# Performance work log

Measured on AMD Instinct MI355X. Metric: run time of the kernel, lower is better.

The kernel has to match this reference:

```python
import jax, jax.numpy as jnp
import numpy as np

TAPS = 5
DELAY = 3
ITERATIONS = 2
EPS = 1e-10


def wpe_one_iteration(Y, power, taps=TAPS, delay=DELAY, eps=EPS):
    """One WPE iteration.
    Y: (B, F, C, T) complex STFT signal.
    power: (B, F, T) real power estimate.
    Returns dereverberated signal, same shape as Y.
    """
    B, F, C, T = Y.shape
    inv_pow = 1.0 / jnp.maximum(power, eps)  # (B,F,T)

    # Tap-delayed (Toeplitz-like) stacked signal: Ytil[..., p, d, t] = Y[..., d, t - delay - p]
    Ytil = jnp.stack(
        [jnp.pad(Y[..., : T - delay - p], ((0, 0), (0, 0), (0, 0), (delay + p, 0)))
         for p in range(taps)],
        axis=2,
    )  # (B, F, taps, C, T)

    # Original implementation only accumulates statistics for frames where the
    # full tap window is available: t >= delay + taps - 1.
    valid = (jnp.arange(T) >= delay + taps - 1).astype(power.dtype)
    w = inv_pow * valid  # (B,F,T)

    Psi_w = jnp.conj(Ytil) * w[:, :, None, None, :]  # (B,F,taps,C,T)

    # Power-weighted covariance matrix R[(p,d),(q,e)] and cross-correlation b[(p,d),e]
    R = jnp.einsum('bfpdt,bfqet->bfpdqe', Psi_w, Ytil).reshape(B, F, taps * C, taps * C)
    b = jnp.einsum('bfpdt,bfet->bfpde', Psi_w, Y).reshape(B, F, taps * C, C)

    eye = jnp.eye(taps * C, dtype=R.dtype)
    # Batched per-frequency linear solve for the conjugate filter matrix
    G_conj = jnp.linalg.solve(R + eps * eye, b).reshape(B, F, taps, C, C)

    # reverb tail: sum over taps p and source channels d
    reverb_tail = jnp.einsum('bfpde,bfpdt->bfet', G_conj, Ytil)
    return Y - reverb_tail


def setup_inputs() -> dict:
    key = jax.random.key(0)
    k1, k2 = jax.random.split(key)
    B, T, C, F = 8, 512, 8, 257
    data_real = jax.random.normal(k1, (B, T, C, F), dtype=jnp.float32)
    data_imag = jax.random.normal(k2, (B, T, C, F), dtype=jnp.float32)
    ilens = jnp.full((B,), T, dtype=jnp.int64)
    return {"data_real": data_real, "data_imag": data_imag, "ilens": ilens}


def reference(data_real, data_imag, ilens):
    # data: (B, T, C, F) -> (B, F, C, T)
    data = (data_real + 1j * data_imag).astype(jnp.complex64)
    Y = jnp.transpose(data, (0, 3, 2, 1))  # (B,F,C,T)
    enhanced = Y
    for _ in range(ITERATIONS):
        power = jnp.mean(enhanced.real ** 2 + enhanced.imag ** 2, axis=-2)  # (B,F,T)
        enhanced = wpe_one_iteration(Y, power)
        # NOTE: original code calls `enhanced.masked_fill(...)` (non in-place),
        # whose result is discarded -> it is a no-op; ilens here are all == T anyway.
    enhanced = jnp.transpose(enhanced, (0, 3, 2, 1))  # (B,T,C,F)
    # Return real/imag stacked so output is a real float tensor (B,T,C,F,2)
    return jnp.stack([enhanced.real, enhanced.imag], axis=-1)
```

## Files before the change

kernel.cpp:

```cpp
#include <hip/hip_runtime.h>

constexpr int BB = 8;
constexpr int TT = 512;
constexpr int CHN = 8;
constexpr int FF = 257;
constexpr int TAPS = 5;
constexpr int DELAY = 3;
constexpr int NBF = BB * FF;
constexpr int ROWQ = 20;
constexpr int MC = 48;
constexpr int RS = 98;

typedef short s8v __attribute__((ext_vector_type(8)));
typedef float f4  __attribute__((ext_vector_type(4)));

__global__ void k_pack(const float* __restrict__ re, const float* __restrict__ im,
                       float* __restrict__ Yg, float* __restrict__ pw) {
  const int ft = blockIdx.x, tt = blockIdx.y, b = blockIdx.z;
  const int f0 = ft * 32, t0 = tt * 16;
  __shared__ float ls[32 * 258];
  const int tid = threadIdx.x;
  const int l = tid & 31;
  const int r = tid >> 5;
  const int f = f0 + l;
  if (f < FF) {
    for (int k = 0; k < 32; ++k) {
      const int task = r + 8 * k;
      const int ri = task & 1;
      const int c  = (task >> 1) & 7;
      const int t  = task >> 4;
      const float* src = ri ? im : re;
      const float v = src[(((size_t)b * TT + t0 + t) * CHN + c) * FF + f];
      ls[l * 258 + (t * 16 + c * 2 + ri)] = v;
    }
  }
  __syncthreads();
  for (int ff = 0; ff < 32; ++ff) {
    const int fg = f0 + ff;
    if (fg >= FF) break;
    Yg[(((size_t)b * FF + fg) * TT + t0) * 16 + tid] = ls[ff * 258 + tid];
  }
  if (f < FF) {
#pragma unroll
    for (int s = 0; s < 2; ++s) {
      const int t = (tid >> 5) + 8 * s;
      const float* row = &ls[l * 258 + t * 16];
      float ss = 0.f;
#pragma unroll
      for (int q = 0; q < 8; ++q) {
        const float2 v = *(const float2*)&row[q * 2];
        ss += v.x * v.x + v.y * v.y;
      }
      pw[((size_t)b * FF + f) * TT + t0 + t] = ss * (1.0f / CHN);
    }
  }
}

__device__ __forceinline__ unsigned bf16rn(float x) {
  unsigned b = __float_as_uint(x);
  return (b + 0x7fffu + ((b >> 16) & 1u)) >> 16;
}

__global__ __launch_bounds__(384, 4)
void k_corr(const float* __restrict__ Yg,
            const float* __restrict__ pw,
            float2* __restrict__ Mg) {
  const int bf = blockIdx.x;
  __shared__ float pre[512 * 9];
  __shared__ float pim[512 * 9];
  __shared__ unsigned short tiles[4 * 1920];
  const int tid = threadIdx.x;

  for (int t = tid; t < TT; t += 384) {
    const float p = pw[(size_t)bf * TT + t];
    pre[t * 9 + 8] = (t >= DELAY + TAPS - 1) ? rsqrtf(fmaxf(p, 1e-10f)) : 0.0f;
  }
  const float4* ybase4 = (const float4*)(Yg + (size_t)bf * TT * 16);
  for (int fi = tid; fi < TT * 4; fi += 384) {
    const int t = fi >> 2, q = fi & 3;
    const float4 v = ybase4[fi];
    pre[t * 9 + 2 * q] = v.x; pre[t * 9 + 2 * q + 1] = v.z;
    pim[t * 9 + 2 * q] = v.y; pim[t * 9 + 2 * q + 1] = v.w;
  }
  __syncthreads();

  const int lane = tid & 63, wv = tid >> 6;
  const int rt = (wv < 3) ? 0 : (wv < 5 ? 1 : 2);
  const int ct = (wv < 3) ? wv : (wv < 5 ? wv - 2 : 2);
  const int lr = lane & 15, lk = lane >> 4;
  const int aoff = (rt * 16 + lr) * 40 + lk * 8;
  const int boff = (ct * 16 + lr) * 40 + lk * 8;

  f4 accre  = {0.f, 0.f, 0.f, 0.f};
  f4 accim1 = {0.f, 0.f, 0.f, 0.f};
  f4 accim2 = {0.f, 0.f, 0.f, 0.f};

  for (int kt = 0; kt < 16; ++kt) {
    const int kt0 = kt * 32;
#pragma unroll
    for (int cc = 0; cc < 2; ++cc) {
      const int c = tid + cc * 384;
      const int kp = c & 15, row = c >> 4;
      const int t = kt0 + 2 * kp;
      const int sh = (row < 40) ? (DELAY + (row >> 3)) : 0;
      const int e  = (row < 40) ? (row & 7) : (row - 40);
      int s0 = t - sh;     if (s0 < 0) s0 = 0;
      int s1 = t + 1 - sh; if (s1 < 0) s1 = 0;
      const float u0 = pre[t * 9 + 8], u1 = pre[(t + 1) * 9 + 8];
      const float v0r = u0 * pre[s0 * 9 + e], v0i = u0 * pim[s0 * 9 + e];
      const float v1r = u1 * pre[s1 * 9 + e], v1i = u1 * pim[s1 * 9 + e];
      const int idx = row * 40 + 2 * kp;
      {
        const unsigned b0 = __float_as_uint(v0r), b1 = __float_as_uint(v1r);
        *(unsigned*)&tiles[idx] = (b0 >> 16) | (b1 & 0xffff0000u);
        *(unsigned*)&tiles[1920 + idx] =
            bf16rn(v0r - __uint_as_float(b0 & 0xffff0000u)) |
            (bf16rn(v1r - __uint_as_float(b1 & 0xffff0000u)) << 16);
      }
      {
        const unsigned b0 = __float_as_uint(v0i), b1 = __float_as_uint(v1i);
        *(unsigned*)&tiles[3840 + idx] = (b0 >> 16) | (b1 & 0xffff0000u);
        *(unsigned*)&tiles[5760 + idx] =
            bf16rn(v0i - __uint_as_float(b0 & 0xffff0000u)) |
            (bf16rn(v1i - __uint_as_float(b1 & 0xffff0000u)) << 16);
      }
    }
    __syncthreads();
    const s8v crhA = *(const s8v*)&tiles[aoff];
    const s8v crlA = *(const s8v*)&tiles[1920 + aoff];
    const s8v cihA = *(const s8v*)&tiles[3840 + aoff];
    const s8v cilA = *(const s8v*)&tiles[5760 + aoff];
    const s8v crhB = *(const s8v*)&tiles[boff];
    const s8v crlB = *(const s8v*)&tiles[1920 + boff];
    const s8v cihB = *(const s8v*)&tiles[3840 + boff];
    const s8v cilB = *(const s8v*)&tiles[5760 + boff];
    accre  = __builtin_amdgcn_mfma_f32_16x16x32_bf16(crhA, crhB, accre, 0, 0, 0);
    accre  = __builtin_amdgcn_mfma_f32_16x16x32_bf16(crlA, crhB, accre, 0, 0, 0);
    accre  = __builtin_amdgcn_mfma_f32_16x16x32_bf16(crhA, crlB, accre, 0, 0, 0);
    accre  = __builtin_amdgcn_mfma_f32_16x16x32_bf16(cihA, cihB, accre, 0, 0, 0);
    accre  = __builtin_amdgcn_mfma_f32_16x16x32_bf16(cilA, cihB, accre, 0, 0, 0);
    accre  = __builtin_amdgcn_mfma_f32_16x16x32_bf16(cihA, cilB, accre, 0, 0, 0);
    accim1 = __builtin_amdgcn_mfma_f32_16x16x32_bf16(crhA, cihB, accim1, 0, 0, 0);
    accim1 = __builtin_amdgcn_mfma_f32_16x16x32_bf16(crlA, cihB, accim1, 0, 0, 0);
    accim1 = __builtin_amdgcn_mfma_f32_16x16x32_bf16(crhA, cilB, accim1, 0, 0, 0);
    accim2 = __builtin_amdgcn_mfma_f32_16x16x32_bf16(cihA, crhB, accim2, 0, 0, 0);
    accim2 = __builtin_amdgcn_mfma_f32_16x16x32_bf16(cilA, crhB, accim2, 0, 0, 0);
    accim2 = __builtin_amdgcn_mfma_f32_16x16x32_bf16(cihA, crlB, accim2, 0, 0, 0);
    __syncthreads();
  }

#pragma unroll
  for (int r = 0; r < 4; ++r) {
    const int i = rt * 16 + lk * 4 + r;
    const int j = ct * 16 + lr;
    const float revl = accre[r];
    const float imvl = accim1[r] - accim2[r];
    if (i < 40) {
      float rr = revl;
      if (i == j) rr += 1e-10f;
      Mg[((size_t)bf * 40 + i) * MC + j] = make_float2(rr, imvl);
    }
    if (rt < ct && j < 40) {
      Mg[((size_t)bf * 40 + j) * MC + i] = make_float2(revl, -imvl);
    }
  }
}

__global__ __launch_bounds__(128) void k_solve(const float2* __restrict__ Mg,
                                               float2* __restrict__ Gg) {
  const int bf = blockIdx.x;
  __shared__ float ml[40 * RS];
  const int tid = threadIdx.x;
  for (int idx = tid; idx < 40 * MC; idx += 128) {
    const int i = idx / MC, j = idx - i * MC;
    float2 v = Mg[((size_t)bf * 40 + i) * MC + j];
    *(float2*)&ml[i * RS + j * 2] = v;
  }
  __syncthreads();
  const int li = tid >> 3, lj = tid & 7;
  for (int k = 0; k < 40; ++k) {
    const float inr = __builtin_amdgcn_rcpf(ml[k * RS + k * 2]);
    for (int i = k + 1 + li; i < 40; i += 16) {
      const float2 aik = *(float2*)&ml[i * RS + k * 2];
      const float fr = aik.x * inr;
      const float fi = aik.y * inr;
      for (int j = k + 1 + lj; j < MC; j += 8) {
        const float2 ak = *(float2*)&ml[k * RS + j * 2];
        float2 ai = *(float2*)&ml[i * RS + j * 2];
        ai.x -= fr * ak.x - fi * ak.y;
        ai.y -= fr * ak.y + fi * ak.x;
        *(float2*)&ml[i * RS + j * 2] = ai;
      }
    }
    __syncthreads();
  }
  const int lane = tid & 63, wave = tid >> 6;
  const int e = 4 * wave + (lane & 3), cc = lane >> 2;
  for (int k = 39; k >= 0; --k) {
    float sr = 0.f, si = 0.f;
    for (int j = k + 1 + cc; j < 40; j += 16) {
      const float2 u = *(float2*)&ml[k * RS + j * 2];
      const float2 x = *(float2*)&ml[j * RS + (40 + e) * 2];
      sr += u.x * x.x - u.y * x.y;
      si += u.x * x.y + u.y * x.x;
    }
    sr += __shfl_xor(sr, 4);  si += __shfl_xor(si, 4);
    sr += __shfl_xor(sr, 8);  si += __shfl_xor(si, 8);
    sr += __shfl_xor(sr, 16); si += __shfl_xor(si, 16);
    sr += __shfl_xor(sr, 32); si += __shfl_xor(si, 32);
    if (cc == 0) {
      const float inr = __builtin_amdgcn_rcpf(ml[k * RS + k * 2]);
      const float2 rhs = *(float2*)&ml[k * RS + (40 + e) * 2];
      *(float2*)&ml[k * RS + (40 + e) * 2] =
          make_float2((rhs.x - sr) * inr, (rhs.y - si) * inr);
    }
    asm volatile("" ::: "memory");
  }
  __syncthreads();
  for (int idx = tid; idx < 320; idx += 128) {
    const int i = idx >> 3, ee = idx & 7;
    Gg[(size_t)bf * 320 + idx] = *(float2*)&ml[i * RS + (40 + ee) * 2];
  }
}

template <int MODE>
__global__ __launch_bounds__(256) void k_tail(float* __restrict__ Yg,
                                              const float2* __restrict__ Gg,
                                              float* __restrict__ pw) {
  const int bf = blockIdx.x;
  __shared__ float yl[TT * ROWQ];
  __shared__ float gl[640];
  const int tid = threadIdx.x;
  for (int idx = tid; idx < 320; idx += 256) {
    float2 g = Gg[(size_t)bf * 320 + idx];
    *(float2*)&gl[idx * 2] = g;
  }
  const float4* ybase4 = (const float4*)(Yg + (size_t)bf * TT * 16);
  for (int fi = tid; fi < TT * 4; fi += 256) {
    const int row = fi >> 2, wq = fi & 3;
    *((float4*)&yl[row * ROWQ + wq * 4]) = ybase4[fi];
  }
  __syncthreads();

  const int t0 = tid;
  const int t1 = tid + 256;
  float acc[2][16];
  {
    const float* yr0 = &yl[t0 * ROWQ];
    const float* yr1 = &yl[t1 * ROWQ];
#pragma unroll
    for (int q = 0; q < 16; ++q) { acc[0][q] = yr0[q]; acc[1][q] = yr1[q]; }
  }
#pragma unroll 1
  for (int p = 0; p < TAPS; ++p) {
    const int rp0 = t0 - DELAY - p;
    const int rp1 = t1 - DELAY - p;
    const float* yrow0 = &yl[(rp0 >= 0 ? rp0 : 0) * ROWQ];
    const float* yrow1 = &yl[rp1 * ROWQ];
    const float m0 = (rp0 >= 0) ? 1.0f : 0.0f;
    const float* gp = &gl[p * 128];
#pragma unroll
    for (int d = 0; d < CHN; ++d) {
      const float y0r = m0 * yrow0[2 * d], y0i = m0 * yrow0[2 * d + 1];
      const float y1r = yrow1[2 * d],      y1i = yrow1[2 * d + 1];
      const float4 g0 = *(const float4*)&gp[d * 16 + 0];
      const float4 g1 = *(const float4*)&gp[d * 16 + 4];
      const float4 g2 = *(const float4*)&gp[d * 16 + 8];
      const float4 g3 = *(const float4*)&gp[d * 16 + 12];
      const float gr[8] = {g0.x, g0.z, g1.x, g1.z, g2.x, g2.z, g3.x, g3.z};
      const float gi[8] = {g0.y, g0.w, g1.y, g1.w, g2.y, g2.w, g3.y, g3.w};
#pragma unroll
      for (int ee = 0; ee < 8; ++ee) {
        acc[0][2 * ee]     -= gr[ee] * y0r - gi[ee] * y0i;
        acc[0][2 * ee + 1] -= gr[ee] * y0i + gi[ee] * y0r;
        acc[1][2 * ee]     -= gr[ee] * y1r - gi[ee] * y1i;
        acc[1][2 * ee + 1] -= gr[ee] * y1i + gi[ee] * y1r;
      }
    }
  }
  float* ybase = Yg + (size_t)bf * TT * 16;
  if (MODE == 0) {
#pragma unroll
    for (int s = 0; s < 2; ++s) {
      const int t = tid + s * 256;
      float ss = 0.f;
#pragma unroll
      for (int q = 0; q < 16; ++q) ss += acc[s][q] * acc[s][q];
      pw[(size_t)bf * TT + t] = ss * (1.0f / CHN);
    }
  } else {
#pragma unroll
    for (int s = 0; s < 2; ++s) {
      const int t = tid + s * 256;
      float4* dst = (float4*)(ybase + (size_t)t * 16);
      dst[0] = make_float4(acc[s][0], acc[s][1], acc[s][2], acc[s][3]);
      dst[1] = make_float4(acc[s][4], acc[s][5], acc[s][6], acc[s][7]);
      dst[2] = make_float4(acc[s][8], acc[s][9], acc[s][10], acc[s][11]);
      dst[3] = make_float4(acc[s][12], acc[s][13], acc[s][14], acc[s][15]);
    }
  }
}

__global__ void k_unpack(const float* __restrict__ Yg, float* __restrict__ out) {
  const int ft = blockIdx.x, tt = blockIdx.y, b = blockIdx.z;
  const int f0 = ft * 32, t0 = tt * 16;
  __shared__ float ls[32 * 258];
  const int tid = threadIdx.x;
  for (int ff = 0; ff < 32; ++ff) {
    const int fg = f0 + ff;
    if (fg >= FF) break;
    ls[ff * 258 + tid] = Yg[(((size_t)b * FF + fg) * TT + t0) * 16 + tid];
  }
  __syncthreads();
  const int l = tid & 31, r = tid >> 5;
  const int fg = f0 + l;
  if (fg < FF) {
    for (int k = 0; k < 16; ++k) {
      const int task = r + 8 * k;
      const int t = task >> 3, c = task & 7;
      const float2 v = *(float2*)&ls[l * 258 + t * 16 + c * 2];
      *(float2*)&out[((((size_t)b * TT + t0 + t) * CHN + c) * FF + fg) * 2] = v;
    }
  }
}

extern "C" void kernel_launch(void* const* d_in, const int* in_sizes, int n_in,
                              void* d_out, int out_size, void* d_ws, size_t ws_size,
                              hipStream_t stream) {
  const float* re = (const float*)d_in[0];
  const float* im = (const float*)d_in[1];
  float* ws = (float*)d_ws;

  float*  Yg = ws;
  float*  pw = Yg + (size_t)NBF * TT * 16;
  float2* Mg = (float2*)(pw + (size_t)NBF * TT);
  float2* Gg = Mg + (size_t)NBF * 40 * MC;
  float*  out = (float*)d_out;

  const dim3 gridT(9, 32, BB);
  k_pack<<<gridT, 256, 0, stream>>>(re, im, Yg, pw);

  for (int iter = 0; iter < 2; ++iter) {
    k_corr<<<NBF, 384, 0, stream>>>(Yg, pw, Mg);
    k_solve<<<NBF, 128, 0, stream>>>(Mg, Gg);
    if (iter == 0)
      k_tail<0><<<NBF, 256, 0, stream>>>(Yg, Gg, pw);
    else
      k_tail<1><<<NBF, 256, 0, stream>>>(Yg, Gg, pw);
  }

  k_unpack<<<gridT, 256, 0, stream>>>(Yg, out);
}
```

Before: 480.0 us.

## Double-buffer correlation tiles and run the solve with a single wave

The correlation kernel now uses two LDS tile buffers and builds the next K-slice while the MFMAs consume the current one, so each iteration needs one barrier instead of two. Its launch-bounds occupancy hint is also dropped. The solve kernel shrinks to one 64-thread wavefront, which lets the per-pivot block barriers become compiler memory fences, with the shuffle reduction adjusted to match. The costs are more LDS per correlation block, possibly lower occupancy, and half as many threads doing the elimination work.

```diff
diff --git a/kernel.cpp b/kernel.cpp
--- a/kernel.cpp
+++ b/kernel.cpp
@@ -61,14 +61,14 @@
   return (b + 0x7fffu + ((b >> 16) & 1u)) >> 16;
 }
 
-__global__ __launch_bounds__(384, 4)
+__global__ __launch_bounds__(384)
 void k_corr(const float* __restrict__ Yg,
             const float* __restrict__ pw,
             float2* __restrict__ Mg) {
   const int bf = blockIdx.x;
   __shared__ float pre[512 * 9];
   __shared__ float pim[512 * 9];
-  __shared__ unsigned short tiles[4 * 1920];
+  __shared__ unsigned short tiles[2 * 7680];
   const int tid = threadIdx.x;
 
   for (int t = tid; t < TT; t += 384) {
@@ -82,21 +82,8 @@
     pre[t * 9 + 2 * q] = v.x; pre[t * 9 + 2 * q + 1] = v.z;
     pim[t * 9 + 2 * q] = v.y; pim[t * 9 + 2 * q + 1] = v.w;
   }
-  __syncthreads();
-
-  const int lane = tid & 63, wv = tid >> 6;
-  const int rt = (wv < 3) ? 0 : (wv < 5 ? 1 : 2);
-  const int ct = (wv < 3) ? wv : (wv < 5 ? wv - 2 : 2);
-  const int lr = lane & 15, lk = lane >> 4;
-  const int aoff = (rt * 16 + lr) * 40 + lk * 8;
-  const int boff = (ct * 16 + lr) * 40 + lk * 8;
-
-  f4 accre  = {0.f, 0.f, 0.f, 0.f};
-  f4 accim1 = {0.f, 0.f, 0.f, 0.f};
-  f4 accim2 = {0.f, 0.f, 0.f, 0.f};
-
-  for (int kt = 0; kt < 16; ++kt) {
-    const int kt0 = kt * 32;
+
+  auto build = [&](int kt0, unsigned short* tb) {
 #pragma unroll
     for (int cc = 0; cc < 2; ++cc) {
       const int c = tid + cc * 384;
@@ -112,28 +99,46 @@
       const int idx = row * 40 + 2 * kp;
       {
         const unsigned b0 = __float_as_uint(v0r), b1 = __float_as_uint(v1r);
-        *(unsigned*)&tiles[idx] = (b0 >> 16) | (b1 & 0xffff0000u);
-        *(unsigned*)&tiles[1920 + idx] =
+        *(unsigned*)&tb[idx] = (b0 >> 16) | (b1 & 0xffff0000u);
+        *(unsigned*)&tb[1920 + idx] =
             bf16rn(v0r - __uint_as_float(b0 & 0xffff0000u)) |
             (bf16rn(v1r - __uint_as_float(b1 & 0xffff0000u)) << 16);
       }
       {
         const unsigned b0 = __float_as_uint(v0i), b1 = __float_as_uint(v1i);
-        *(unsigned*)&tiles[3840 + idx] = (b0 >> 16) | (b1 & 0xffff0000u);
-        *(unsigned*)&tiles[5760 + idx] =
+        *(unsigned*)&tb[3840 + idx] = (b0 >> 16) | (b1 & 0xffff0000u);
+        *(unsigned*)&tb[5760 + idx] =
             bf16rn(v0i - __uint_as_float(b0 & 0xffff0000u)) |
             (bf16rn(v1i - __uint_as_float(b1 & 0xffff0000u)) << 16);
       }
     }
-    __syncthreads();
-    const s8v crhA = *(const s8v*)&tiles[aoff];
-    const s8v crlA = *(const s8v*)&tiles[1920 + aoff];
-    const s8v cihA = *(const s8v*)&tiles[3840 + aoff];
-    const s8v cilA = *(const s8v*)&tiles[5760 + aoff];
-    const s8v crhB = *(const s8v*)&tiles[boff];
-    const s8v crlB = *(const s8v*)&tiles[1920 + boff];
-    const s8v cihB = *(const s8v*)&tiles[3840 + boff];
-    const s8v cilB = *(const s8v*)&tiles[5760 + boff];
+  };
+
+  __syncthreads();
+  build(0, tiles);
+  __syncthreads();
+
+  const int lane = tid & 63, wv = tid >> 6;
+  const int rt = (wv < 3) ? 0 : (wv < 5 ? 1 : 2);
+  const int ct = (wv < 3) ? wv : (wv < 5 ? wv - 2 : 2);
+  const int lr = lane & 15, lk = lane >> 4;
+  const int aoff = (rt * 16 + lr) * 40 + lk * 8;
+  const int boff = (ct * 16 + lr) * 40 + lk * 8;
+
+  f4 accre  = {0.f, 0.f, 0.f, 0.f};
+  f4 accim1 = {0.f, 0.f, 0.f, 0.f};
+  f4 accim2 = {0.f, 0.f, 0.f, 0.f};
+
+  for (int kt = 0; kt < 16; ++kt) {
+    const unsigned short* cur = tiles + (kt & 1) * 7680;
+    const s8v crhA = *(const s8v*)&cur[aoff];
+    const s8v crlA = *(const s8v*)&cur[1920 + aoff];
+    const s8v cihA = *(const s8v*)&cur[3840 + aoff];
+    const s8v cilA = *(const s8v*)&cur[5760 + aoff];
+    const s8v crhB = *(const s8v*)&cur[boff];
+    const s8v crlB = *(const s8v*)&cur[1920 + boff];
+    const s8v cihB = *(const s8v*)&cur[3840 + boff];
+    const s8v cilB = *(const s8v*)&cur[5760 + boff];
     accre  = __builtin_amdgcn_mfma_f32_16x16x32_bf16(crhA, crhB, accre, 0, 0, 0);
     accre  = __builtin_amdgcn_mfma_f32_16x16x32_bf16(crlA, crhB, accre, 0, 0, 0);
     accre  = __builtin_amdgcn_mfma_f32_16x16x32_bf16(crhA, crlB, accre, 0, 0, 0);
@@ -146,6 +151,7 @@
     accim2 = __builtin_amdgcn_mfma_f32_16x16x32_bf16(cihA, crhB, accim2, 0, 0, 0);
     accim2 = __builtin_amdgcn_mfma_f32_16x16x32_bf16(cilA, crhB, accim2, 0, 0, 0);
     accim2 = __builtin_amdgcn_mfma_f32_16x16x32_bf16(cihA, crlB, accim2, 0, 0, 0);
+    if (kt < 15) build((kt + 1) * 32, tiles + ((kt + 1) & 1) * 7680);
     __syncthreads();
   }
 
@@ -166,21 +172,21 @@
   }
 }
 
-__global__ __launch_bounds__(128) void k_solve(const float2* __restrict__ Mg,
-                                               float2* __restrict__ Gg) {
+__global__ __launch_bounds__(64) void k_solve(const float2* __restrict__ Mg,
+                                              float2* __restrict__ Gg) {
   const int bf = blockIdx.x;
   __shared__ float ml[40 * RS];
-  const int tid = threadIdx.x;
-  for (int idx = tid; idx < 40 * MC; idx += 128) {
+  const int lane = threadIdx.x;
+  for (int idx = lane; idx < 40 * MC; idx += 64) {
     const int i = idx / MC, j = idx - i * MC;
     float2 v = Mg[((size_t)bf * 40 + i) * MC + j];
     *(float2*)&ml[i * RS + j * 2] = v;
   }
   __syncthreads();
-  const int li = tid >> 3, lj = tid & 7;
+  const int li = lane >> 3, lj = lane & 7;
   for (int k = 0; k < 40; ++k) {
     const float inr = __builtin_amdgcn_rcpf(ml[k * RS + k * 2]);
-    for (int i = k + 1 + li; i < 40; i += 16) {
+    for (int i = k + 1 + li; i < 40; i += 8) {
       const float2 aik = *(float2*)&ml[i * RS + k * 2];
       const float fr = aik.x * inr;
       const float fi = aik.y * inr;
@@ -192,19 +198,17 @@
         *(float2*)&ml[i * RS + j * 2] = ai;
       }
     }
-    __syncthreads();
-  }
-  const int lane = tid & 63, wave = tid >> 6;
-  const int e = 4 * wave + (lane & 3), cc = lane >> 2;
+    asm volatile("" ::: "memory");
+  }
+  const int e = lane & 7, cc = lane >> 3;
   for (int k = 39; k >= 0; --k) {
     float sr = 0.f, si = 0.f;
-    for (int j = k + 1 + cc; j < 40; j += 16) {
+    for (int j = k + 1 + cc; j < 40; j += 8) {
       const float2 u = *(float2*)&ml[k * RS + j * 2];
       const float2 x = *(float2*)&ml[j * RS + (40 + e) * 2];
       sr += u.x * x.x - u.y * x.y;
       si += u.x * x.y + u.y * x.x;
     }
-    sr += __shfl_xor(sr, 4);  si += __shfl_xor(si, 4);
     sr += __shfl_xor(sr, 8);  si += __shfl_xor(si, 8);
     sr += __shfl_xor(sr, 16); si += __shfl_xor(si, 16);
     sr += __shfl_xor(sr, 32); si += __shfl_xor(si, 32);
@@ -217,7 +221,7 @@
     asm volatile("" ::: "memory");
   }
   __syncthreads();
-  for (int idx = tid; idx < 320; idx += 128) {
+  for (int idx = lane; idx < 320; idx += 64) {
     const int i = idx >> 3, ee = idx & 7;
     Gg[(size_t)bf * 320 + idx] = *(float2*)&ml[i * RS + (40 + ee) * 2];
   }
@@ -342,7 +346,7 @@
 
   for (int iter = 0; iter < 2; ++iter) {
     k_corr<<<NBF, 384, 0, stream>>>(Yg, pw, Mg);
-    k_solve<<<NBF, 128, 0, stream>>>(Mg, Gg);
+    k_solve<<<NBF, 64, 0, stream>>>(Mg, Gg);
     if (iter == 0)
       k_tail<0><<<NBF, 256, 0, stream>>>(Yg, Gg, pw);
     else
```

Result: slower. 561.4 us (+16.9%).

## Fuse per-frequency linear solve into reverb-tail kernel with prefetched Y

Applied to the files above, without the earlier changes.

Merges the separate solve kernel into the tail kernel, so the filter matrix stays in shared memory instead of going through a global Gg buffer. One kernel launch per iteration is removed. The global loads of the Y tile are issued into registers before the elimination starts, so their latency overlaps the solve. The solve now runs with 256 threads and a wider row and column split. The cost is higher shared-memory and register use per block, which may reduce occupancy.

```diff
diff --git a/kernel.cpp b/kernel.cpp
--- a/kernel.cpp
+++ b/kernel.cpp
@@ -166,21 +166,32 @@
   }
 }
 
-__global__ __launch_bounds__(128) void k_solve(const float2* __restrict__ Mg,
-                                               float2* __restrict__ Gg) {
+template <int MODE>
+__global__ __launch_bounds__(256) void k_tailsolve(float* __restrict__ Yg,
+                                                   const float2* __restrict__ Mg,
+                                                   float* __restrict__ pw) {
   const int bf = blockIdx.x;
+  __shared__ float yl[TT * ROWQ];
   __shared__ float ml[40 * RS];
+  __shared__ float gl[640];
   const int tid = threadIdx.x;
-  for (int idx = tid; idx < 40 * MC; idx += 128) {
+
+  const float4* ybase4 = (const float4*)(Yg + (size_t)bf * TT * 16);
+  float4 stage[8];
+#pragma unroll
+  for (int s = 0; s < 8; ++s) stage[s] = ybase4[tid + s * 256];
+
+  for (int idx = tid; idx < 40 * MC; idx += 256) {
     const int i = idx / MC, j = idx - i * MC;
     float2 v = Mg[((size_t)bf * 40 + i) * MC + j];
     *(float2*)&ml[i * RS + j * 2] = v;
   }
   __syncthreads();
+
   const int li = tid >> 3, lj = tid & 7;
   for (int k = 0; k < 40; ++k) {
     const float inr = __builtin_amdgcn_rcpf(ml[k * RS + k * 2]);
-    for (int i = k + 1 + li; i < 40; i += 16) {
+    for (int i = k + 1 + li; i < 40; i += 32) {
       const float2 aik = *(float2*)&ml[i * RS + k * 2];
       const float fr = aik.x * inr;
       const float fi = aik.y * inr;
@@ -194,51 +205,42 @@
     }
     __syncthreads();
   }
-  const int lane = tid & 63, wave = tid >> 6;
-  const int e = 4 * wave + (lane & 3), cc = lane >> 2;
-  for (int k = 39; k >= 0; --k) {
-    float sr = 0.f, si = 0.f;
-    for (int j = k + 1 + cc; j < 40; j += 16) {
-      const float2 u = *(float2*)&ml[k * RS + j * 2];
-      const float2 x = *(float2*)&ml[j * RS + (40 + e) * 2];
-      sr += u.x * x.x - u.y * x.y;
-      si += u.x * x.y + u.y * x.x;
-    }
-    sr += __shfl_xor(sr, 4);  si += __shfl_xor(si, 4);
-    sr += __shfl_xor(sr, 8);  si += __shfl_xor(si, 8);
-    sr += __shfl_xor(sr, 16); si += __shfl_xor(si, 16);
-    sr += __shfl_xor(sr, 32); si += __shfl_xor(si, 32);
-    if (cc == 0) {
-      const float inr = __builtin_amdgcn_rcpf(ml[k * RS + k * 2]);
-      const float2 rhs = *(float2*)&ml[k * RS + (40 + e) * 2];
-      *(float2*)&ml[k * RS + (40 + e) * 2] =
-          make_float2((rhs.x - sr) * inr, (rhs.y - si) * inr);
-    }
-    asm volatile("" ::: "memory");
-  }
-  __syncthreads();
-  for (int idx = tid; idx < 320; idx += 128) {
+
+  const int lane = tid & 63, wv = tid >> 6;
+  {
+    const int e = 2 * wv + (lane & 1), cc = lane >> 1;
+    for (int k = 39; k >= 0; --k) {
+      float sr = 0.f, si = 0.f;
+      for (int j = k + 1 + cc; j < 40; j += 32) {
+        const float2 u = *(float2*)&ml[k * RS + j * 2];
+        const float2 x = *(float2*)&ml[j * RS + (40 + e) * 2];
+        sr += u.x * x.x - u.y * x.y;
+        si += u.x * x.y + u.y * x.x;
+      }
+      sr += __shfl_xor(sr, 2);  si += __shfl_xor(si, 2);
+      sr += __shfl_xor(sr, 4);  si += __shfl_xor(si, 4);
+      sr += __shfl_xor(sr, 8);  si += __shfl_xor(si, 8);
+      sr += __shfl_xor(sr, 16); si += __shfl_xor(si, 16);
+      sr += __shfl_xor(sr, 32); si += __shfl_xor(si, 32);
+      if (cc == 0) {
+        const float inr = __builtin_amdgcn_rcpf(ml[k * RS + k * 2]);
+        const float2 rhs = *(float2*)&ml[k * RS + (40 + e) * 2];
+        *(float2*)&ml[k * RS + (40 + e) * 2] =
+            make_float2((rhs.x - sr) * inr, (rhs.y - si) * inr);
+      }
+      asm volatile("" ::: "memory");
+    }
+  }
+  __syncthreads();
+
+  for (int idx = tid; idx < 320; idx += 256) {
     const int i = idx >> 3, ee = idx & 7;
-    Gg[(size_t)bf * 320 + idx] = *(float2*)&ml[i * RS + (40 + ee) * 2];
-  }
-}
-
-template <int MODE>
-__global__ __launch_bounds__(256) void k_tail(float* __restrict__ Yg,
-                                              const float2* __restrict__ Gg,
-                                              float* __restrict__ pw) {
-  const int bf = blockIdx.x;
-  __shared__ float yl[TT * ROWQ];
-  __shared__ float gl[640];
-  const int tid = threadIdx.x;
-  for (int idx = tid; idx < 320; idx += 256) {
-    float2 g = Gg[(size_t)bf * 320 + idx];
-    *(float2*)&gl[idx * 2] = g;
-  }
-  const float4* ybase4 = (const float4*)(Yg + (size_t)bf * TT * 16);
-  for (int fi = tid; fi < TT * 4; fi += 256) {
-    const int row = fi >> 2, wq = fi & 3;
-    *((float4*)&yl[row * ROWQ + wq * 4]) = ybase4[fi];
+    *(float2*)&gl[idx * 2] = *(float2*)&ml[i * RS + (40 + ee) * 2];
+  }
+#pragma unroll
+  for (int s = 0; s < 8; ++s) {
+    const int fi = tid + s * 256;
+    *((float4*)&yl[(fi >> 2) * ROWQ + (fi & 3) * 4]) = stage[s];
   }
   __syncthreads();
 
@@ -334,7 +336,6 @@
   float*  Yg = ws;
   float*  pw = Yg + (size_t)NBF * TT * 16;
   float2* Mg = (float2*)(pw + (size_t)NBF * TT);
-  float2* Gg = Mg + (size_t)NBF * 40 * MC;
   float*  out = (float*)d_out;
 
   const dim3 gridT(9, 32, BB);
@@ -342,11 +343,10 @@
 
   for (int iter = 0; iter < 2; ++iter) {
     k_corr<<<NBF, 384, 0, stream>>>(Yg, pw, Mg);
-    k_solve<<<NBF, 128, 0, stream>>>(Mg, Gg);
     if (iter == 0)
-      k_tail<0><<<NBF, 256, 0, stream>>>(Yg, Gg, pw);
+      k_tailsolve<0><<<NBF, 256, 0, stream>>>(Yg, Mg, pw);
     else
-      k_tail<1><<<NBF, 256, 0, stream>>>(Yg, Gg, pw);
+      k_tailsolve<1><<<NBF, 256, 0, stream>>>(Yg, Mg, pw);
   }
 
   k_unpack<<<gridT, 256, 0, stream>>>(Yg, out);
```

Measured after the change: 698.8 us. +45.6%, slower.
